# Kernel tuning notes

Hardware: AMD Instinct MI355X
Metric: run time of the kernel (lower is better)

The kernel has to match this reference:

```python
import jax, jax.numpy as jnp
import numpy as np

SQRT2 = 1.4142135623730951
MH_C = 0.8673250705840776  # (2/sqrt(3)) * pi**(-1/4), mexican-hat normalizer


def _bn(x, eps=1e-5):
    # BatchNorm (training-mode batch stats, default affine gamma=1, beta=0)
    mu = jnp.mean(x, axis=0, keepdims=True)
    var = jnp.var(x, axis=0, keepdims=True)
    return (x - mu) / jnp.sqrt(var + eps)


def setup_inputs() -> dict:
    key = jax.random.key(0)
    ks = jax.random.split(key, 10)
    N, F, E, B, OUT = 1024, 1024, 32768, 16, 10
    H = F // 2  # 512 after Haar DWT
    x = jax.random.normal(ks[0], (N, F), dtype=jnp.float32)
    edge_index = jax.random.randint(ks[1], (2, E), 0, N, dtype=jnp.int32)
    batch = jnp.sort(jax.random.randint(ks[2], (N,), 0, B, dtype=jnp.int32))
    w_att = jax.random.normal(ks[3], (2,), dtype=jnp.float32)  # Linear(2,1,bias=False)
    wk_scale = jnp.ones((H, H), dtype=jnp.float32)
    wk_trans = jax.random.normal(ks[4], (H, H), dtype=jnp.float32) * 0.1
    wk_wav_w = jax.random.normal(ks[5], (H, H), dtype=jnp.float32) * 0.05
    wk_base_w = jax.random.normal(ks[6], (H, H), dtype=jnp.float32) * 0.05
    fc1_w = jax.random.normal(ks[7], (512, F + H), dtype=jnp.float32) * 0.02
    fc1_b = jnp.zeros((512,), dtype=jnp.float32)
    fc2_w = jax.random.normal(ks[8], (OUT, 512), dtype=jnp.float32) * 0.02
    fc2_b = jnp.zeros((OUT,), dtype=jnp.float32)
    return {"x": x, "w_att": w_att, "wk_scale": wk_scale, "wk_trans": wk_trans,
            "wk_wav_w": wk_wav_w, "wk_base_w": wk_base_w, "fc1_w": fc1_w,
            "fc1_b": fc1_b, "fc2_w": fc2_w, "fc2_b": fc2_b,
            "edge_index": edge_index, "batch": batch, "num_graphs": B}


def reference(x, w_att, wk_scale, wk_trans, wk_wav_w, wk_base_w,
              fc1_w, fc1_b, fc2_w, fc2_b, edge_index, batch, num_graphs):
    N = x.shape[0]
    # --- WaveletAttention: Haar ('db1') DWT over the feature dim ---
    xe, xo = x[:, 0::2], x[:, 1::2]
    low = (xe + xo) / SQRT2            # [N, 512]
    high = (xe - xo) / SQRT2           # [N, 512]
    scores = jax.nn.sigmoid(low * w_att[0] + high * w_att[1])
    h = scores * low + (1.0 - scores) * high
    # --- GINConv aggregation (eps=0): self + sum of neighbor features ---
    src, dst = edge_index[0], edge_index[1]
    agg = h + jax.ops.segment_sum(h[src], dst, num_segments=N)  # [N, 512]
    # --- WavKAN layer 512->512 (mexican hat) ---
    xs = (agg[:, None, :] - wk_trans) / wk_scale                # [N, 512, 512]
    xs2 = xs * xs
    mh = MH_C * (1.0 - xs2) * jnp.exp(-0.5 * xs2)
    wav = jnp.einsum('noi,oi->no', mh, wk_wav_w)                # [N, 512]
    base = jax.nn.silu(agg) @ wk_base_w.T
    conv_out = _bn(wav + base)   # WavKAN-internal BatchNorm1d
    conv_out = _bn(conv_out)     # bn1 (dropout p=0 -> identity)
    # --- skip concat + bn2 ---
    z = _bn(jnp.concatenate([x, conv_out], axis=1))             # [N, 1536]
    # --- global mean pool over graphs ---
    sums = jax.ops.segment_sum(z, batch, num_segments=num_graphs)
    cnts = jax.ops.segment_sum(jnp.ones((N,), z.dtype), batch, num_segments=num_graphs)
    pooled = sums / jnp.maximum(cnts, 1.0)[:, None]             # [B, 1536]
    # --- classifier head (eval-mode dropout = identity) ---
    h1 = jax.nn.relu(pooled @ fc1_w.T + fc1_b)
    return h1 @ fc2_w.T + fc2_b
```

## Files before the change

### kernel.cpp

```cpp
#include <hip/hip_runtime.h>
#include <math.h>

#define N_NODES 1024
#define F_DIM   1024
#define H_DIM   512
#define E_EDGES 32768
#define B_GRAPHS 16
#define OUT_DIM 10
#define FH_DIM  1536
#define EPS 1e-5f
#define MH_C_D 0.8673250705840776
#define C2_D   0.72134752044448170368
#define C2_F   ((float)C2_D)
#define CSC    0.84932180028801904272f
#define WC2F   ((float)(MH_C_D / C2_D))
#define INV_SQRT2 0.70710678118654752440f

typedef float v2f __attribute__((ext_vector_type(2)));
typedef unsigned int u32;
typedef const __attribute__((address_space(1))) u32 gu32;
typedef __attribute__((address_space(3))) u32 lu32;

#if __has_builtin(__builtin_amdgcn_exp2f)
#define EXP2NEG(x) __builtin_amdgcn_exp2f(-(x))
#else
#define EXP2NEG(x) __expf(-0.69314718055994530942f * (x))
#endif

#define PK_FMA_BB(d, a, p) \
    asm("v_pk_fma_f32 %0, %1, %2, %2 op_sel:[0,0,1] op_sel_hi:[1,0,1]" \
        : "=v"(d) : "v"(a), "v"(p))
#define PK_MUL2(d, a, b) \
    asm("v_pk_mul_f32 %0, %1, %2" : "=v"(d) : "v"(a), "v"(b))
#define PK_WZC(d, s, k) \
    asm("v_pk_mul_f32 %0, %1, %2 op_sel:[0,0] op_sel_hi:[0,1]" \
        : "=v"(d) : "v"(s), "v"(k))
#define PK_FMA_HI_ACC(acc, s, p) \
    asm("v_pk_fma_f32 %0, %1, %2, %0 op_sel:[0,1,0] op_sel_hi:[1,1,1]" \
        : "+v"(acc) : "v"(s), "v"(p))

__global__ __launch_bounds__(256) void k_setup(const float* __restrict__ x,
                                               const float* __restrict__ watt,
                                               float* __restrict__ h,
                                               const float* __restrict__ scale,
                                               const float* __restrict__ trans,
                                               const float* __restrict__ ww,
                                               const float* __restrict__ bw,
                                               float* __restrict__ pk,
                                               float* __restrict__ zbase) {
    const int bid = blockIdx.x;
    const int t = threadIdx.x;
    if (bid < 2048) {
        int idx = bid * 256 + t;
        float2 p = ((const float2*)x)[idx];
        float lo = (p.x + p.y) * INV_SQRT2;
        float hi = (p.x - p.y) * INV_SQRT2;
        float tt = lo * watt[0] + hi * watt[1];
        float sc = 1.0f / (1.0f + __expf(-tt));
        h[idx] = sc * lo + (1.0f - sc) * hi;
    } else if (bid < 3072) {
        int g = (bid - 2048) * 256 + t;
        float iv = 1.0f / scale[g];
        float4 p;
        p.x = iv * CSC;
        p.y = -(trans[g] * iv * CSC);
        p.z = -(ww[g] * WC2F);
        p.w = bw[g];
        ((float4*)pk)[g] = p;
    } else {
        zbase[(bid - 3072) * 256 + t] = 0.0f;
    }
}

__global__ __launch_bounds__(256) void k_hx(const int* __restrict__ dst,
                                            int* __restrict__ deg,
                                            const float* __restrict__ x,
                                            float* __restrict__ xsum,
                                            float* __restrict__ xsum2) {
    const int bid = blockIdx.x;
    const int t = threadIdx.x;
    if (bid < 128) {
        int e = bid * 256 + t;
        atomicAdd(&deg[dst[e]], 1);
    } else {
        const int n0 = (bid - 128) * 16;
        float s[4] = {}, s2[4] = {};
        for (int r = 0; r < 16; ++r) {
            #pragma unroll
            for (int ch = 0; ch < 4; ++ch) {
                float v = x[(n0 + r) * F_DIM + ch * 256 + t];
                s[ch] += v; s2[ch] += v * v;
            }
        }
        #pragma unroll
        for (int ch = 0; ch < 4; ++ch) {
            unsafeAtomicAdd(&xsum[ch * 256 + t], s[ch]);
            unsafeAtomicAdd(&xsum2[ch * 256 + t], s2[ch]);
        }
    }
}

__global__ __launch_bounds__(1024) void k_scan(const int* __restrict__ deg,
                                               int* __restrict__ start,
                                               int* __restrict__ cursor) {
    __shared__ int wsum[16];
    int t = threadIdx.x;
    int lane = t & 63, wid = t >> 6;
    int v = deg[t];
    int x = v;
    #pragma unroll
    for (int off = 1; off < 64; off <<= 1) {
        int y = __shfl_up(x, off, 64);
        if (lane >= off) x += y;
    }
    if (lane == 63) wsum[wid] = x;
    __syncthreads();
    if (t < 16) {
        int w = wsum[t];
        int xs = w;
        #pragma unroll
        for (int off = 1; off < 16; off <<= 1) {
            int y = __shfl_up(xs, off, 64);
            if (t >= off) xs += y;
        }
        wsum[t] = xs - w;
    }
    __syncthreads();
    int excl = wsum[wid] + x - v;
    start[t] = excl;
    cursor[t] = excl;
}

__global__ __launch_bounds__(256) void k_fill(const int* __restrict__ src,
                                              const int* __restrict__ dst,
                                              int* __restrict__ cursor,
                                              int* __restrict__ elist) {
    int e = blockIdx.x * 256 + threadIdx.x;
    int slot = atomicAdd(&cursor[dst[e]], 1);
    elist[slot] = src[e];
}

__global__ __launch_bounds__(256) void k_gather(const float* __restrict__ h,
                                                const int* __restrict__ start,
                                                const int* __restrict__ deg,
                                                const int* __restrict__ elist,
                                                float* __restrict__ agg) {
    int d = blockIdx.x;
    int t = threadIdx.x;
    int st = start[d], dg = deg[d];
    const float2* h2 = (const float2*)h;
    float2 a = h2[d * 256 + t];
    int k = 0;
    for (; k + 4 <= dg; k += 4) {
        int s0 = elist[st + k];
        int s1 = elist[st + k + 1];
        int s2 = elist[st + k + 2];
        int s3 = elist[st + k + 3];
        float2 v0 = h2[s0 * 256 + t];
        float2 v1 = h2[s1 * 256 + t];
        float2 v2 = h2[s2 * 256 + t];
        float2 v3 = h2[s3 * 256 + t];
        a.x += (v0.x + v1.x) + (v2.x + v3.x);
        a.y += (v0.y + v1.y) + (v2.y + v3.y);
    }
    for (; k < dg; ++k) {
        int s0 = elist[st + k];
        float2 v0 = h2[s0 * 256 + t];
        a.x += v0.x; a.y += v0.y;
    }
    ((float2*)agg)[d * 256 + t] = a;
}

__global__ __launch_bounds__(256) void k_transpose(const float* __restrict__ agg,
                                                   float* __restrict__ aggT,
                                                   float* __restrict__ siluT) {
    __shared__ float tile[64 * 65];
    const int t = threadIdx.x;
    const int n0 = blockIdx.x * 64;
    const int i0 = blockIdx.y * 64;
    #pragma unroll
    for (int v = 0; v < 4; ++v) {
        int flat = v * 256 + t;
        int r = flat >> 4, c4 = flat & 15;
        float4 a = *(const float4*)&agg[(n0 + r) * H_DIM + i0 + c4 * 4];
        tile[(c4 * 4 + 0) * 65 + r] = a.x;
        tile[(c4 * 4 + 1) * 65 + r] = a.y;
        tile[(c4 * 4 + 2) * 65 + r] = a.z;
        tile[(c4 * 4 + 3) * 65 + r] = a.w;
    }
    __syncthreads();
    #pragma unroll
    for (int v = 0; v < 4; ++v) {
        int flat = v * 256 + t;
        int il = flat >> 4, c4 = flat & 15;
        float4 a;
        a.x = tile[il * 65 + c4 * 4 + 0];
        a.y = tile[il * 65 + c4 * 4 + 1];
        a.z = tile[il * 65 + c4 * 4 + 2];
        a.w = tile[il * 65 + c4 * 4 + 3];
        int g = (i0 + il) * N_NODES + n0 + c4 * 4;
        *(float4*)&aggT[g] = a;
        float4 s;
        s.x = a.x / (1.0f + __expf(-a.x));
        s.y = a.y / (1.0f + __expf(-a.y));
        s.z = a.z / (1.0f + __expf(-a.z));
        s.w = a.w / (1.0f + __expf(-a.w));
        *(float4*)&siluT[g] = s;
    }
}

#define TN 64
#define TO 32
#define KI 16
#define TOP (TO + 1)
#define ZSPLIT 4
#define ZLEN (H_DIM / ZSPLIT)
#define NSTG (ZLEN / KI)
__global__ __launch_bounds__(256) void k_wavelet(const float* __restrict__ aggT,
                                                 const float* __restrict__ siluT,
                                                 const float* __restrict__ pk,
                                                 float* __restrict__ vbp) {
    __shared__ float sA[2][KI * TN];
    __shared__ float sS[2][KI * TN];
    __shared__ float4 sP4[2][KI * TOP];

    const int t  = threadIdx.x;
    const int n0 = blockIdx.x * TN;
    const int o0 = blockIdx.y * TO;
    const int z0 = blockIdx.z * ZLEN;
    const int nl = (t & 15) * 4;
    const int ol = (t >> 4) * 2;

    const int po  = t >> 4;
    const int pii = t & 15;
    const float4* pk4 = (const float4*)pk;

    v2f accw[2][2] = {};
    v2f accb[2][2] = {};
    v2f kC2; kC2.x = 1.0f; kC2.y = -C2_F;

    {
        int g = (z0 + (t >> 4)) * N_NODES + n0 + nl;
        __builtin_amdgcn_global_load_lds((gu32*)&aggT[g],  (lu32*)&sA[0][t * 4], 16, 0, 0);
        __builtin_amdgcn_global_load_lds((gu32*)&siluT[g], (lu32*)&sS[0][t * 4], 16, 0, 0);
        float4 r0 = pk4[(size_t)(o0 + po) * H_DIM + z0 + pii];
        float4 r1 = pk4[(size_t)(o0 + po + 16) * H_DIM + z0 + pii];
        sP4[0][pii * TOP + po]      = r0;
        sP4[0][pii * TOP + po + 16] = r1;
    }
    __syncthreads();

    for (int stg = 0; stg < NSTG; ++stg) {
        const int i0 = z0 + stg * KI;
        const int nb = (stg + 1) & 1;
        float4 r0, r1;
        if (stg + 1 < NSTG) {
            int g = (i0 + KI + (t >> 4)) * N_NODES + n0 + nl;
            __builtin_amdgcn_global_load_lds((gu32*)&aggT[g],  (lu32*)&sA[nb][t * 4], 16, 0, 0);
            __builtin_amdgcn_global_load_lds((gu32*)&siluT[g], (lu32*)&sS[nb][t * 4], 16, 0, 0);
            r0 = pk4[(size_t)(o0 + po) * H_DIM + i0 + KI + pii];
            r1 = pk4[(size_t)(o0 + po + 16) * H_DIM + i0 + KI + pii];
        }
        const float*  pA = sA[stg & 1];
        const float*  pS = sS[stg & 1];
        const float4* pP = sP4[stg & 1];
        #pragma unroll 4
        for (int ii = 0; ii < KI; ++ii) {
            float4 af = *(const float4*)&pA[ii * TN + nl];
            float4 sf = *(const float4*)&pS[ii * TN + nl];
            v2f a01 = {af.x, af.y}, a23 = {af.z, af.w};
            v2f s01 = {sf.x, sf.y}, s23 = {sf.z, sf.w};
            #pragma unroll
            for (int oo = 0; oo < 2; ++oo) {
                float4 pq = pP[ii * TOP + ol + oo];
                v2f pxy = {pq.x, pq.y};
                v2f pzw = {pq.z, pq.w};
                v2f wzc; PK_WZC(wzc, pzw, kC2);
                v2f y0;  PK_FMA_BB(y0, a01, pxy);
                v2f y1;  PK_FMA_BB(y1, a23, pxy);
                v2f q0;  PK_MUL2(q0, y0, y0);
                v2f q1;  PK_MUL2(q1, y1, y1);
                v2f w0;  PK_FMA_BB(w0, q0, wzc);
                v2f w1;  PK_FMA_BB(w1, q1, wzc);
                float e00 = EXP2NEG(q0.x), e01 = EXP2NEG(q0.y);
                float e10 = EXP2NEG(q1.x), e11 = EXP2NEG(q1.y);
                accw[oo][0].x += w0.x * e00;
                accw[oo][0].y += w0.y * e01;
                accw[oo][1].x += w1.x * e10;
                accw[oo][1].y += w1.y * e11;
                PK_FMA_HI_ACC(accb[oo][0], s01, pzw);
                PK_FMA_HI_ACC(accb[oo][1], s23, pzw);
            }
        }
        if (stg + 1 < NSTG) {
            sP4[nb][pii * TOP + po]      = r0;
            sP4[nb][pii * TOP + po + 16] = r1;
        }
        __syncthreads();
    }
    float* out = vbp + (size_t)blockIdx.z * (N_NODES * H_DIM);
    #pragma unroll
    for (int nn = 0; nn < 4; ++nn) {
        int pr = nn >> 1, cmu = nn & 1;
        float2 o2;
        o2.x = cmu ? accw[0][pr].y + accb[0][pr].y : accw[0][pr].x + accb[0][pr].x;
        o2.y = cmu ? accw[1][pr].y + accb[1][pr].y : accw[1][pr].x + accb[1][pr].x;
        *(float2*)&out[(n0 + nl + nn) * H_DIM + o0 + ol] = o2;
    }
}

__global__ __launch_bounds__(256) void k_reduce(const float* __restrict__ vbp,
                                                float* __restrict__ vb,
                                                float* __restrict__ colsum,
                                                float* __restrict__ colsum2) {
    const int b = blockIdx.x;
    const int o0 = (b & 7) * 64;
    const int n0 = (b >> 3) * 64;
    const int t = threadIdx.x;
    const int oc = o0 + (t & 63);
    const int nsub = t >> 6;
    float s = 0.f, s2 = 0.f;
    for (int r = 0; r < 16; ++r) {
        int n = n0 + r * 4 + nsub;
        size_t idx = (size_t)n * H_DIM + oc;
        float v = 0.f;
        #pragma unroll
        for (int z = 0; z < ZSPLIT; ++z) v += vbp[z * (N_NODES * H_DIM) + idx];
        vb[idx] = v;
        s += v; s2 += v * v;
    }
    __shared__ float sh1[256], sh2[256];
    sh1[t] = s; sh2[t] = s2;
    __syncthreads();
    if (t < 64) {
        s  = sh1[t] + sh1[t + 64] + sh1[t + 128] + sh1[t + 192];
        s2 = sh2[t] + sh2[t + 64] + sh2[t + 128] + sh2[t + 192];
        unsafeAtomicAdd(&colsum[o0 + t], s);
        unsafeAtomicAdd(&colsum2[o0 + t], s2);
    }
}

__global__ __launch_bounds__(256) void k_pool(const float* __restrict__ x,
                                              const float* __restrict__ vb,
                                              const int* __restrict__ batch,
                                              const float* __restrict__ colsum,
                                              const float* __restrict__ colsum2,
                                              const float* __restrict__ xsum,
                                              const float* __restrict__ xsum2,
                                              float* __restrict__ pooled) {
    const int b = blockIdx.x;
    const int ch = blockIdx.y;
    const int t = threadIdx.x;

    __shared__ int s_cnt[4];
    __shared__ int s_st;
    int c = 0;
    for (int n = t; n < N_NODES; n += 256) {
        int bb = batch[n];
        int pb = (n == 0) ? -1 : batch[n - 1];
        c += (bb == b) ? 1 : 0;
        if (bb == b && pb != b) s_st = n;
    }
    #pragma unroll
    for (int off = 32; off > 0; off >>= 1) c += __shfl_down(c, off);
    if ((t & 63) == 0) s_cnt[t >> 6] = c;
    __syncthreads();
    int cnt = s_cnt[0] + s_cnt[1] + s_cnt[2] + s_cnt[3];
    int st = (cnt > 0) ? s_st : 0;
    float ic = (cnt > 0) ? 1.0f / (float)cnt : 0.f;

    float acc = 0.f;
    if (ch < 4) {
        int col = ch * 256 + t;
        float mu  = xsum[col] * (1.0f / N_NODES);
        float var = xsum2[col] * (1.0f / N_NODES) - mu * mu;
        if (var < 0.f) var = 0.f;
        float S = 1.0f / sqrtf(var + EPS);
        const float* base = x + col;
        for (int r = 0; r < cnt; ++r) acc += base[(size_t)(st + r) * F_DIM];
        pooled[b * FH_DIM + col] = (acc * ic - mu) * S;
    } else {
        int col = (ch - 4) * 256 + t;
        float mu  = colsum[col] * (1.0f / N_NODES);
        float var = colsum2[col] * (1.0f / N_NODES) - mu * mu;
        if (var < 0.f) var = 0.f;
        float s1v = 1.0f / sqrtf(var + EPS);
        float v1  = var * s1v * s1v;
        float s2v = 1.0f / sqrtf(v1 + EPS);
        float v2  = v1 * s2v * s2v;
        float s3v = 1.0f / sqrtf(v2 + EPS);
        float S = s1v * s2v * s3v;
        const float* base = vb + col;
        for (int r = 0; r < cnt; ++r) acc += base[(size_t)(st + r) * H_DIM];
        pooled[b * FH_DIM + F_DIM + col] = (acc * ic - mu) * S;
    }
}

__global__ __launch_bounds__(256) void k_fc1(const float* __restrict__ pooled,
                                             const float* __restrict__ w,
                                             const float* __restrict__ bias,
                                             float* __restrict__ h1) {
    int wid = (blockIdx.x * 256 + threadIdx.x) >> 6;
    int lane = threadIdx.x & 63;
    int b = wid >> 9, o = wid & 511;
    const float4* pr = (const float4*)(pooled + b * FH_DIM);
    const float4* wr = (const float4*)(w + o * FH_DIM);
    float acc = 0.f;
    #pragma unroll
    for (int k = 0; k < 6; ++k) {
        float4 a = pr[k * 64 + lane];
        float4 v = wr[k * 64 + lane];
        acc += a.x * v.x + a.y * v.y + a.z * v.z + a.w * v.w;
    }
    #pragma unroll
    for (int off = 32; off > 0; off >>= 1) acc += __shfl_down(acc, off);
    if (lane == 0) h1[b * H_DIM + o] = fmaxf(acc + bias[o], 0.f);
}

__global__ __launch_bounds__(256) void k_fc2(const float* __restrict__ h1,
                                             const float* __restrict__ w,
                                             const float* __restrict__ bias,
                                             float* __restrict__ outp) {
    int wid = (blockIdx.x * 256 + threadIdx.x) >> 6;
    int lane = threadIdx.x & 63;
    if (wid >= B_GRAPHS * OUT_DIM) return;
    int b = wid / OUT_DIM, u = wid % OUT_DIM;
    const float4* hr = (const float4*)(h1 + b * H_DIM);
    const float4* wr = (const float4*)(w + u * H_DIM);
    float acc = 0.f;
    #pragma unroll
    for (int k = 0; k < 2; ++k) {
        float4 a = hr[k * 64 + lane];
        float4 v = wr[k * 64 + lane];
        acc += a.x * v.x + a.y * v.y + a.z * v.z + a.w * v.w;
    }
    #pragma unroll
    for (int off = 32; off > 0; off >>= 1) acc += __shfl_down(acc, off);
    if (lane == 0) outp[b * OUT_DIM + u] = acc + bias[u];
}

extern "C" void kernel_launch(void* const* d_in, const int* in_sizes, int n_in,
                              void* d_out, int out_size, void* d_ws, size_t ws_size,
                              hipStream_t stream) {
    const float* x       = (const float*)d_in[0];
    const float* w_att   = (const float*)d_in[1];
    const float* wk_scale= (const float*)d_in[2];
    const float* wk_trans= (const float*)d_in[3];
    const float* wk_wav  = (const float*)d_in[4];
    const float* wk_base = (const float*)d_in[5];
    const float* fc1_w   = (const float*)d_in[6];
    const float* fc1_b   = (const float*)d_in[7];
    const float* fc2_w   = (const float*)d_in[8];
    const float* fc2_b   = (const float*)d_in[9];
    const int*   eidx    = (const int*)d_in[10];
    const int*   batch   = (const int*)d_in[11];
    float* outp = (float*)d_out;

    float* ws = (float*)d_ws;
    const int NH = N_NODES * H_DIM;
    float* h      = ws;
    float* agg    = h + NH;
    float* aggT   = agg + NH;
    float* siluT  = aggT + NH;
    float* pk     = siluT + NH;
    float* vbp    = pk + 4 * (H_DIM * H_DIM);
    float* vb     = vbp + (size_t)ZSPLIT * NH;
    float* colsum = vb + NH;
    float* colsum2= colsum + 512;
    float* xsum   = colsum2 + 512;
    float* xsum2  = xsum + 1024;
    int*   deg    = (int*)(xsum2 + 1024);
    int*   estart = deg + N_NODES;
    int*   cursor = estart + N_NODES;
    int*   elist  = cursor + N_NODES;
    float* pooled = (float*)(elist + E_EDGES);
    float* h1     = pooled + B_GRAPHS * FH_DIM;

    const int* src = eidx;
    const int* dst = eidx + E_EDGES;

    k_setup<<<3088, 256, 0, stream>>>(x, w_att, h, wk_scale, wk_trans, wk_wav, wk_base,
                                      pk, colsum);
    k_hx<<<192, 256, 0, stream>>>(dst, deg, x, xsum, xsum2);
    k_scan<<<1, N_NODES, 0, stream>>>(deg, estart, cursor);
    k_fill<<<E_EDGES / 256, 256, 0, stream>>>(src, dst, cursor, elist);
    k_gather<<<N_NODES, 256, 0, stream>>>(h, estart, deg, elist, agg);
    {
        dim3 grid(N_NODES / 64, H_DIM / 64);
        k_transpose<<<grid, 256, 0, stream>>>(agg, aggT, siluT);
    }
    {
        dim3 grid(N_NODES / TN, H_DIM / TO, ZSPLIT);
        k_wavelet<<<grid, 256, 0, stream>>>(aggT, siluT, pk, vbp);
    }
    k_reduce<<<128, 256, 0, stream>>>(vbp, vb, colsum, colsum2);
    {
        dim3 grid(B_GRAPHS, 6);
        k_pool<<<grid, 256, 0, stream>>>(x, vb, batch, colsum, colsum2, xsum, xsum2, pooled);
    }
    k_fc1<<<(B_GRAPHS * H_DIM * 64) / 256, 256, 0, stream>>>(pooled, fc1_w, fc1_b, h1);
    k_fc2<<<(B_GRAPHS * OUT_DIM * 64 + 255) / 256, 256, 0, stream>>>(h1, fc2_w, fc2_b, outp);
}
```

Baseline: 196.6 us.

## Widen wavelet node tile, double K-split, move weight packing into k_hx

The wavelet kernel's node tile doubles from 64 to 128, so each thread now computes 8 nodes × 2 outputs. This reuses each LDS weight read across more work and adds independent exp/FMA chains for ILP. The reduction dimension is split 8 ways instead of 4, which keeps the block count the same. In exchange, the partial-sum buffer that k_reduce must read doubles, and register pressure per thread rises. Weight packing also moves from k_setup into k_hx, which rebalances those two launches.

```diff
diff --git a/kernel.cpp b/kernel.cpp
--- a/kernel.cpp
+++ b/kernel.cpp
@@ -42,11 +42,6 @@
 __global__ __launch_bounds__(256) void k_setup(const float* __restrict__ x,
                                                const float* __restrict__ watt,
                                                float* __restrict__ h,
-                                               const float* __restrict__ scale,
-                                               const float* __restrict__ trans,
-                                               const float* __restrict__ ww,
-                                               const float* __restrict__ bw,
-                                               float* __restrict__ pk,
                                                float* __restrict__ zbase) {
     const int bid = blockIdx.x;
     const int t = threadIdx.x;
@@ -58,17 +53,8 @@
         float tt = lo * watt[0] + hi * watt[1];
         float sc = 1.0f / (1.0f + __expf(-tt));
         h[idx] = sc * lo + (1.0f - sc) * hi;
-    } else if (bid < 3072) {
-        int g = (bid - 2048) * 256 + t;
-        float iv = 1.0f / scale[g];
-        float4 p;
-        p.x = iv * CSC;
-        p.y = -(trans[g] * iv * CSC);
-        p.z = -(ww[g] * WC2F);
-        p.w = bw[g];
-        ((float4*)pk)[g] = p;
     } else {
-        zbase[(bid - 3072) * 256 + t] = 0.0f;
+        zbase[(bid - 2048) * 256 + t] = 0.0f;
     }
 }
 
@@ -76,13 +62,18 @@
                                             int* __restrict__ deg,
                                             const float* __restrict__ x,
                                             float* __restrict__ xsum,
-                                            float* __restrict__ xsum2) {
+                                            float* __restrict__ xsum2,
+                                            const float* __restrict__ scale,
+                                            const float* __restrict__ trans,
+                                            const float* __restrict__ ww,
+                                            const float* __restrict__ bw,
+                                            float* __restrict__ pk) {
     const int bid = blockIdx.x;
     const int t = threadIdx.x;
     if (bid < 128) {
         int e = bid * 256 + t;
         atomicAdd(&deg[dst[e]], 1);
-    } else {
+    } else if (bid < 192) {
         const int n0 = (bid - 128) * 16;
         float s[4] = {}, s2[4] = {};
         for (int r = 0; r < 16; ++r) {
@@ -97,6 +88,15 @@
             unsafeAtomicAdd(&xsum[ch * 256 + t], s[ch]);
             unsafeAtomicAdd(&xsum2[ch * 256 + t], s2[ch]);
         }
+    } else {
+        int g = (bid - 192) * 256 + t;
+        float iv = 1.0f / scale[g];
+        float4 p;
+        p.x = iv * CSC;
+        p.y = -(trans[g] * iv * CSC);
+        p.z = -(ww[g] * WC2F);
+        p.w = bw[g];
+        ((float4*)pk)[g] = p;
     }
 }
 
@@ -209,40 +209,44 @@
     }
 }
 
-#define TN 64
+#define TN 128
 #define TO 32
 #define KI 16
 #define TOP (TO + 1)
-#define ZSPLIT 4
+#define ZSPLIT 8
 #define ZLEN (H_DIM / ZSPLIT)
 #define NSTG (ZLEN / KI)
 __global__ __launch_bounds__(256) void k_wavelet(const float* __restrict__ aggT,
                                                  const float* __restrict__ siluT,
                                                  const float* __restrict__ pk,
                                                  float* __restrict__ vbp) {
-    __shared__ float sA[2][KI * TN];
-    __shared__ float sS[2][KI * TN];
+    __shared__ float  sA[2][KI * TN];
+    __shared__ float  sS[2][KI * TN];
     __shared__ float4 sP4[2][KI * TOP];
 
     const int t  = threadIdx.x;
     const int n0 = blockIdx.x * TN;
     const int o0 = blockIdx.y * TO;
     const int z0 = blockIdx.z * ZLEN;
-    const int nl = (t & 15) * 4;
+    const int na = (t & 15) * 4;
     const int ol = (t >> 4) * 2;
 
+    const int srow = t >> 5, scol = (t & 31) * 4;
     const int po  = t >> 4;
     const int pii = t & 15;
     const float4* pk4 = (const float4*)pk;
 
-    v2f accw[2][2] = {};
-    v2f accb[2][2] = {};
+    v2f accw[2][4] = {};
+    v2f accb[2][4] = {};
     v2f kC2; kC2.x = 1.0f; kC2.y = -C2_F;
 
     {
-        int g = (z0 + (t >> 4)) * N_NODES + n0 + nl;
-        __builtin_amdgcn_global_load_lds((gu32*)&aggT[g],  (lu32*)&sA[0][t * 4], 16, 0, 0);
-        __builtin_amdgcn_global_load_lds((gu32*)&siluT[g], (lu32*)&sS[0][t * 4], 16, 0, 0);
+        int g0 = (z0 + srow) * N_NODES + n0 + scol;
+        int g1 = (z0 + 8 + srow) * N_NODES + n0 + scol;
+        __builtin_amdgcn_global_load_lds((gu32*)&aggT[g0],  (lu32*)&sA[0][t * 4], 16, 0, 0);
+        __builtin_amdgcn_global_load_lds((gu32*)&aggT[g1],  (lu32*)&sA[0][1024 + t * 4], 16, 0, 0);
+        __builtin_amdgcn_global_load_lds((gu32*)&siluT[g0], (lu32*)&sS[0][t * 4], 16, 0, 0);
+        __builtin_amdgcn_global_load_lds((gu32*)&siluT[g1], (lu32*)&sS[0][1024 + t * 4], 16, 0, 0);
         float4 r0 = pk4[(size_t)(o0 + po) * H_DIM + z0 + pii];
         float4 r1 = pk4[(size_t)(o0 + po + 16) * H_DIM + z0 + pii];
         sP4[0][pii * TOP + po]      = r0;
@@ -255,9 +259,16 @@
         const int nb = (stg + 1) & 1;
         float4 r0, r1;
         if (stg + 1 < NSTG) {
-            int g = (i0 + KI + (t >> 4)) * N_NODES + n0 + nl;
-            __builtin_amdgcn_global_load_lds((gu32*)&aggT[g],  (lu32*)&sA[nb][t * 4], 16, 0, 0);
-            __builtin_amdgcn_global_load_lds((gu32*)&siluT[g], (lu32*)&sS[nb][t * 4], 16, 0, 0);
+            int g0 = (i0 + KI + srow) * N_NODES + n0 + scol;
+            int g1 = (i0 + KI + 8 + srow) * N_NODES + n0 + scol;
+            __builtin_amdgcn_global_load_lds((gu32*)&aggT[g0],
+                                             (lu32*)&sA[nb][t * 4], 16, 0, 0);
+            __builtin_amdgcn_global_load_lds((gu32*)&aggT[g1],
+                                             (lu32*)&sA[nb][1024 + t * 4], 16, 0, 0);
+            __builtin_amdgcn_global_load_lds((gu32*)&siluT[g0],
+                                             (lu32*)&sS[nb][t * 4], 16, 0, 0);
+            __builtin_amdgcn_global_load_lds((gu32*)&siluT[g1],
+                                             (lu32*)&sS[nb][1024 + t * 4], 16, 0, 0);
             r0 = pk4[(size_t)(o0 + po) * H_DIM + i0 + KI + pii];
             r1 = pk4[(size_t)(o0 + po + 16) * H_DIM + i0 + KI + pii];
         }
@@ -266,30 +277,39 @@
         const float4* pP = sP4[stg & 1];
         #pragma unroll 4
         for (int ii = 0; ii < KI; ++ii) {
-            float4 af = *(const float4*)&pA[ii * TN + nl];
-            float4 sf = *(const float4*)&pS[ii * TN + nl];
-            v2f a01 = {af.x, af.y}, a23 = {af.z, af.w};
-            v2f s01 = {sf.x, sf.y}, s23 = {sf.z, sf.w};
+            float4 af0 = *(const float4*)&pA[ii * TN + na];
+            float4 af1 = *(const float4*)&pA[ii * TN + 64 + na];
+            float4 sf0 = *(const float4*)&pS[ii * TN + na];
+            float4 sf1 = *(const float4*)&pS[ii * TN + 64 + na];
+            v2f a01 = {af0.x, af0.y}, a23 = {af0.z, af0.w};
+            v2f a45 = {af1.x, af1.y}, a67 = {af1.z, af1.w};
+            v2f s01 = {sf0.x, sf0.y}, s23 = {sf0.z, sf0.w};
+            v2f s45 = {sf1.x, sf1.y}, s67 = {sf1.z, sf1.w};
             #pragma unroll
             for (int oo = 0; oo < 2; ++oo) {
                 float4 pq = pP[ii * TOP + ol + oo];
                 v2f pxy = {pq.x, pq.y};
                 v2f pzw = {pq.z, pq.w};
                 v2f wzc; PK_WZC(wzc, pzw, kC2);
-                v2f y0;  PK_FMA_BB(y0, a01, pxy);
-                v2f y1;  PK_FMA_BB(y1, a23, pxy);
-                v2f q0;  PK_MUL2(q0, y0, y0);
-                v2f q1;  PK_MUL2(q1, y1, y1);
-                v2f w0;  PK_FMA_BB(w0, q0, wzc);
-                v2f w1;  PK_FMA_BB(w1, q1, wzc);
-                float e00 = EXP2NEG(q0.x), e01 = EXP2NEG(q0.y);
-                float e10 = EXP2NEG(q1.x), e11 = EXP2NEG(q1.y);
-                accw[oo][0].x += w0.x * e00;
-                accw[oo][0].y += w0.y * e01;
-                accw[oo][1].x += w1.x * e10;
-                accw[oo][1].y += w1.y * e11;
+                v2f y0, y1, y2, y3, q0, q1, q2, q3, w0, w1, w2, w3;
+                PK_FMA_BB(y0, a01, pxy); PK_FMA_BB(y1, a23, pxy);
+                PK_FMA_BB(y2, a45, pxy); PK_FMA_BB(y3, a67, pxy);
+                PK_MUL2(q0, y0, y0); PK_MUL2(q1, y1, y1);
+                PK_MUL2(q2, y2, y2); PK_MUL2(q3, y3, y3);
+                PK_FMA_BB(w0, q0, wzc); PK_FMA_BB(w1, q1, wzc);
+                PK_FMA_BB(w2, q2, wzc); PK_FMA_BB(w3, q3, wzc);
+                accw[oo][0].x += w0.x * EXP2NEG(q0.x);
+                accw[oo][0].y += w0.y * EXP2NEG(q0.y);
+                accw[oo][1].x += w1.x * EXP2NEG(q1.x);
+                accw[oo][1].y += w1.y * EXP2NEG(q1.y);
+                accw[oo][2].x += w2.x * EXP2NEG(q2.x);
+                accw[oo][2].y += w2.y * EXP2NEG(q2.y);
+                accw[oo][3].x += w3.x * EXP2NEG(q3.x);
+                accw[oo][3].y += w3.y * EXP2NEG(q3.y);
                 PK_FMA_HI_ACC(accb[oo][0], s01, pzw);
                 PK_FMA_HI_ACC(accb[oo][1], s23, pzw);
+                PK_FMA_HI_ACC(accb[oo][2], s45, pzw);
+                PK_FMA_HI_ACC(accb[oo][3], s67, pzw);
             }
         }
         if (stg + 1 < NSTG) {
@@ -300,12 +320,15 @@
     }
     float* out = vbp + (size_t)blockIdx.z * (N_NODES * H_DIM);
     #pragma unroll
-    for (int nn = 0; nn < 4; ++nn) {
-        int pr = nn >> 1, cmu = nn & 1;
-        float2 o2;
-        o2.x = cmu ? accw[0][pr].y + accb[0][pr].y : accw[0][pr].x + accb[0][pr].x;
-        o2.y = cmu ? accw[1][pr].y + accb[1][pr].y : accw[1][pr].x + accb[1][pr].x;
-        *(float2*)&out[(n0 + nl + nn) * H_DIM + o0 + ol] = o2;
+    for (int p = 0; p < 4; ++p) {
+        int rn = n0 + ((p & 2) ? 64 : 0) + na + (p & 1) * 2;
+        float2 lo, hi;
+        lo.x = accw[0][p].x + accb[0][p].x;
+        lo.y = accw[1][p].x + accb[1][p].x;
+        hi.x = accw[0][p].y + accb[0][p].y;
+        hi.y = accw[1][p].y + accb[1][p].y;
+        *(float2*)&out[(size_t)rn * H_DIM + o0 + ol]       = lo;
+        *(float2*)&out[(size_t)(rn + 1) * H_DIM + o0 + ol] = hi;
     }
 }
 
@@ -479,9 +502,9 @@
     const int* src = eidx;
     const int* dst = eidx + E_EDGES;
 
-    k_setup<<<3088, 256, 0, stream>>>(x, w_att, h, wk_scale, wk_trans, wk_wav, wk_base,
-                                      pk, colsum);
-    k_hx<<<192, 256, 0, stream>>>(dst, deg, x, xsum, xsum2);
+    k_setup<<<2064, 256, 0, stream>>>(x, w_att, h, colsum);
+    k_hx<<<1216, 256, 0, stream>>>(dst, deg, x, xsum, xsum2,
+                                   wk_scale, wk_trans, wk_wav, wk_base, pk);
     k_scan<<<1, N_NODES, 0, stream>>>(deg, estart, cursor);
     k_fill<<<E_EDGES / 256, 256, 0, stream>>>(src, dst, cursor, elist);
     k_gather<<<N_NODES, 256, 0, stream>>>(h, estart, deg, elist, agg);
```

After: 197.6 us. About the same (+0.5%).
